# Kernel optimization log

Hardware: AMD Instinct MI355X
Metric: run time of the kernel (lower is better)

Reference implementation:

```python
import jax, jax.numpy as jnp
import numpy as np

H = 768      # hidden_size
R = 64       # lora_dim
E = 8        # n_experts
B, S = 8, 2048


def setup_inputs() -> dict:
    key = jax.random.key(0)
    ks = jax.random.split(key, 10)
    s_in = 1.0 / np.sqrt(H)
    s_r = 1.0 / np.sqrt(R)
    return {
        "x": jax.random.normal(ks[0], (B, S, H), dtype=jnp.float32),
        "enc_w": jax.random.uniform(ks[1], (H, R), jnp.float32, -s_in, s_in),
        "enc_b": jax.random.uniform(ks[2], (R,), jnp.float32, -s_in, s_in),
        "sw_w": jax.random.uniform(ks[3], (R, E), jnp.float32, -s_r, s_r),
        "sw_b": jax.random.uniform(ks[4], (E,), jnp.float32, -s_r, s_r),
        "w1": jax.random.uniform(ks[5], (E, H, R), jnp.float32, -s_in, s_in),
        "b1": jax.random.uniform(ks[6], (E, R), jnp.float32, -s_in, s_in),
        "w2": jax.random.uniform(ks[7], (E, R, H), jnp.float32, -s_r, s_r),
        "b2": jax.random.uniform(ks[8], (E, H), jnp.float32, -s_r, s_r),
    }


def reference(x, enc_w, enc_b, sw_w, sw_b, w1, b1, w2, b2):
    b, s, d = x.shape
    xt = x.reshape(-1, d)                                  # [T, H]
    # router: encoder -> switch -> softmax -> top-1
    x_enc = xt @ enc_w + enc_b                             # [T, R]
    route_prob = jax.nn.softmax(x_enc @ sw_w + sw_b, axis=-1)  # [T, E]
    route_prob_max = jnp.max(route_prob, axis=-1)          # [T]
    routes = jnp.argmax(route_prob, axis=-1)               # [T]
    onehot = jax.nn.one_hot(routes, E, dtype=xt.dtype)     # [T, E]
    # dense dispatch: per-(token, expert) LoRA bottleneck; masked combine
    h = jnp.einsum('td,edr->ter', xt, w1) + b1[None]       # [T, E, R]
    h = jax.nn.gelu(h, approximate=False)
    h = h * onehot[..., None]                              # zero non-routed
    out = jnp.einsum('ter,erd->td', h, w2) + onehot @ b2   # [T, H]
    out = out * route_prob_max[:, None]
    return out.reshape(b, s, d)
```

## Files before the change

kernel.cpp:

```cpp
#include <hip/hip_runtime.h>
#include <math.h>

#define HDIM 768
#define RDIM 64
#define NEXP 8
#define NTOK 16384

typedef _Float16 half8 __attribute__((ext_vector_type(8)));
typedef float float4_t __attribute__((ext_vector_type(4)));

__device__ __forceinline__ float gelu_exact(float v) {
    return 0.5f * v * (1.0f + erff(v * 0.70710678118654752440f));
}

__global__ __launch_bounds__(256) void prep_kernel(
    const float* __restrict__ w1, const float* __restrict__ w2,
    const float* __restrict__ enc_w, const float* __restrict__ enc_b,
    const float* __restrict__ sw_w, const float* __restrict__ sw_b,
    _Float16* __restrict__ w1t, _Float16* __restrict__ w2t,
    float* __restrict__ wrt, float* __restrict__ brr)
{
    const int wid = blockIdx.x * 4 + (threadIdx.x >> 6);
    const int lane = threadIdx.x & 63;
    if (wid < 768) {
        const int e = wid / 96, k0 = (wid % 96) * 8;
        half8 o;
        #pragma unroll
        for (int j = 0; j < 8; j++)
            o[j] = (_Float16)w1[((size_t)(e * HDIM + k0 + j)) * RDIM + lane];
        *(half8*)(w1t + ((size_t)(e * RDIM + lane)) * HDIM + k0) = o;
    } else if (wid < 1536) {
        const int id = wid - 768;
        const int e = id / 96, rem = id % 96;
        const int n = (rem >> 3) * 64 + lane, k0 = (rem & 7) * 8;
        half8 o;
        #pragma unroll
        for (int j = 0; j < 8; j++)
            o[j] = (_Float16)w2[((size_t)(e * RDIM + k0 + j)) * HDIM + n];
        *(half8*)(w2t + ((size_t)(e * HDIM + n)) * RDIM + k0) = o;
    } else if (wid < 1632) {
        const int k = (wid - 1536) * 8 + (lane >> 3);
        const int e = lane & 7;
        float s = 0.0f;
        #pragma unroll 16
        for (int r = 0; r < RDIM; r++)
            s += enc_w[(size_t)k * RDIM + r] * sw_w[r * NEXP + e];
        wrt[e * HDIM + k] = s;
    } else if (wid == 1632) {
        if (lane < NEXP) {
            float s = sw_b[lane];
            #pragma unroll 16
            for (int r = 0; r < RDIM; r++)
                s += enc_b[r] * sw_w[r * NEXP + lane];
            brr[lane] = s;
        }
    }
}

__global__ __launch_bounds__(256, 4) void router_kernel(
    const float* __restrict__ x, const float* __restrict__ wrt,
    const float* __restrict__ brr, float* __restrict__ pmax,
    int* __restrict__ counts, int* __restrict__ lists)
{
    __shared__ __align__(16) float wrl[NEXP][772];
    __shared__ int lcnt[NEXP], gbase[NEXP];

    const int tid = threadIdx.x;
    #pragma unroll
    for (int i0 = 0; i0 < 6; i0++) {
        const int i = tid + i0 * 256;
        const int e = i / 192, k4 = (i % 192) * 4;
        *(float4*)&wrl[e][k4] = *(const float4*)(wrt + e * HDIM + k4);
    }
    if (tid < NEXP) lcnt[tid] = 0;
    __syncthreads();

    const int wv = tid >> 6, lane = tid & 63;
    const int e = lane & 7, tslot = lane >> 3;
    const int tok = blockIdx.x * 32 + wv * 8 + tslot;
    const float* xrow = x + (size_t)tok * HDIM;

    float4_t acc4 = {0.0f, 0.0f, 0.0f, 0.0f};
    for (int k0 = 0; k0 < HDIM; k0 += 64) {
        float4 xv[16];
        #pragma unroll
        for (int u = 0; u < 16; u++)
            xv[u] = *(const float4*)(xrow + k0 + u * 4);
        #pragma unroll
        for (int u = 0; u < 16; u++) {
            const float4 w4 = *(const float4*)(&wrl[e][k0 + u * 4]);
            acc4[0] = fmaf(xv[u].x, w4.x, acc4[0]);
            acc4[1] = fmaf(xv[u].y, w4.y, acc4[1]);
            acc4[2] = fmaf(xv[u].z, w4.z, acc4[2]);
            acc4[3] = fmaf(xv[u].w, w4.w, acc4[3]);
        }
    }
    const float logit = (acc4[0] + acc4[1]) + (acc4[2] + acc4[3]) + brr[e];

    float m = logit; int am = e;
    #pragma unroll
    for (int d = 4; d >= 1; d >>= 1) {
        float om = __shfl_xor(m, d, 8);
        int oam  = __shfl_xor(am, d, 8);
        if (om > m || (om == m && oam < am)) { m = om; am = oam; }
    }
    float s = expf(logit - m);
    #pragma unroll
    for (int d = 1; d <= 4; d <<= 1) s += __shfl_xor(s, d, 8);

    int am_s = -1, lp_s = 0;
    if (e == 0) {
        pmax[tok] = 1.0f / s;
        am_s = am;
        lp_s = atomicAdd(&lcnt[am], 1);
    }
    __syncthreads();
    if (tid < NEXP) gbase[tid] = atomicAdd(&counts[tid * 32], lcnt[tid]);
    __syncthreads();
    if (am_s >= 0)
        lists[am_s * NTOK + gbase[am_s] + lp_s] = tok;
}

__global__ __launch_bounds__(256, 4) void mm1_kernel(
    const float* __restrict__ x, const _Float16* __restrict__ w1t,
    const float* __restrict__ b1, const int* __restrict__ counts,
    const int* __restrict__ lists, _Float16* __restrict__ h)
{
    __shared__ __align__(16) float part[4][16][68];

    const int e = blockIdx.x;
    const int cnt = counts[e * 32];
    const int tid = threadIdx.x;
    const int wv = tid >> 6, lane = tid & 63;
    const int q = lane >> 4, c = lane & 15;

    for (int st = blockIdx.y; st * 16 < cnt; st += gridDim.y) {
        const int base = st * 16;
        const int nt = cnt - base;
        const int tA = lists[e * NTOK + base + min(c, nt - 1)];
        const float* xrow = x + (size_t)tA * HDIM + wv * 192;
        const _Float16* wbase = w1t + ((size_t)(e * RDIM + c)) * HDIM + wv * 192 + q * 8;

        float4 xv[12];
        #pragma unroll
        for (int it = 0; it < 6; it++) {
            xv[2 * it]     = *(const float4*)(xrow + it * 32 + q * 8);
            xv[2 * it + 1] = *(const float4*)(xrow + it * 32 + q * 8 + 4);
        }

        float4_t acc[4] = {{0,0,0,0},{0,0,0,0},{0,0,0,0},{0,0,0,0}};
        #pragma unroll
        for (int it = 0; it < 6; it++) {
            const int k0 = it * 32;
            half8 a;
            a[0] = (_Float16)xv[2*it].x;   a[1] = (_Float16)xv[2*it].y;
            a[2] = (_Float16)xv[2*it].z;   a[3] = (_Float16)xv[2*it].w;
            a[4] = (_Float16)xv[2*it+1].x; a[5] = (_Float16)xv[2*it+1].y;
            a[6] = (_Float16)xv[2*it+1].z; a[7] = (_Float16)xv[2*it+1].w;
            #pragma unroll
            for (int nf = 0; nf < 4; nf++) {
                half8 b = *(const half8*)(wbase + (size_t)nf * 16 * HDIM + k0);
                acc[nf] = __builtin_amdgcn_mfma_f32_16x16x32_f16(a, b, acc[nf], 0, 0, 0);
            }
        }

        #pragma unroll
        for (int nf = 0; nf < 4; nf++)
            #pragma unroll
            for (int i = 0; i < 4; i++)
                part[wv][q * 4 + i][nf * 16 + c] = acc[nf][i];
        __syncthreads();

        #pragma unroll
        for (int j = 0; j < 4; j++) {
            const int idx = tid + 256 * j;
            const int row = idx >> 6, r = idx & 63;
            if (row < nt) {
                const int tok = lists[e * NTOK + base + row];
                float v = part[0][row][r] + part[1][row][r] + part[2][row][r]
                        + part[3][row][r] + b1[e * RDIM + r];
                h[(size_t)tok * RDIM + r] = (_Float16)gelu_exact(v);
            }
        }
        __syncthreads();
    }
}

__global__ __launch_bounds__(256, 3) void mm2_kernel(
    const _Float16* __restrict__ h, const _Float16* __restrict__ w2t,
    const float* __restrict__ b2, const float* __restrict__ pmax,
    const int* __restrict__ counts, const int* __restrict__ lists,
    float* __restrict__ out)
{
    const int e = blockIdx.x;
    const int cnt = counts[e * 32];
    const int wv = threadIdx.x >> 6, lane = threadIdx.x & 63;
    const int q = lane >> 4, c = lane & 15;

    const int task = blockIdx.y * 4 + wv;
    const int nch = task % 3;
    const int sidx = task / 3;

    for (int st = sidx; st * 16 < cnt; st += 128) {
        const int base = st * 16;
        const int nt = cnt - base;
        const int tA = lists[e * NTOK + base + min(c, nt - 1)];
        half8 a0 = *(const half8*)(h + (size_t)tA * RDIM + q * 8);
        half8 a1 = *(const half8*)(h + (size_t)tA * RDIM + 32 + q * 8);

        int tokv[4]; float pm[4]; bool ok[4];
        #pragma unroll
        for (int i = 0; i < 4; i++) {
            const int row = q * 4 + i;
            ok[i] = row < nt;
            tokv[i] = lists[e * NTOK + base + min(row, nt - 1)];
            pm[i] = pmax[tokv[i]];
        }

        #pragma unroll 4
        for (int nf = 0; nf < 16; nf++) {
            const int n = nch * 256 + nf * 16 + c;
            const _Float16* wrow = w2t + ((size_t)(e * HDIM + n)) * RDIM;
            half8 b0 = *(const half8*)(wrow + q * 8);
            half8 b1v = *(const half8*)(wrow + 32 + q * 8);
            float4_t acc = {0, 0, 0, 0};
            acc = __builtin_amdgcn_mfma_f32_16x16x32_f16(a0, b0, acc, 0, 0, 0);
            acc = __builtin_amdgcn_mfma_f32_16x16x32_f16(a1, b1v, acc, 0, 0, 0);
            const float b2v = b2[e * HDIM + n];
            #pragma unroll
            for (int i = 0; i < 4; i++) {
                if (ok[i])
                    out[(size_t)tokv[i] * HDIM + n] = (acc[i] + b2v) * pm[i];
            }
        }
    }
}

extern "C" void kernel_launch(void* const* d_in, const int* in_sizes, int n_in,
                              void* d_out, int out_size, void* d_ws, size_t ws_size,
                              hipStream_t stream) {
    const float* x     = (const float*)d_in[0];
    const float* enc_w = (const float*)d_in[1];
    const float* enc_b = (const float*)d_in[2];
    const float* sw_w  = (const float*)d_in[3];
    const float* sw_b  = (const float*)d_in[4];
    const float* w1    = (const float*)d_in[5];
    const float* b1    = (const float*)d_in[6];
    const float* w2    = (const float*)d_in[7];
    const float* b2    = (const float*)d_in[8];
    float* out = (float*)d_out;

    char* p = (char*)d_ws;
    int*      counts = (int*)p;
    float*    pmax   = (float*)(p + 1024);
    int*      lists  = (int*)(p + 66560);
    float*    wrt    = (float*)(p + 590848);
    float*    brr    = (float*)(p + 615424);
    _Float16* w1t    = (_Float16*)(p + 615680);
    _Float16* w2t    = (_Float16*)(p + 1402112);
    _Float16* h      = (_Float16*)(p + 2188544);

    hipMemsetAsync(d_ws, 0, 1024, stream);

    hipLaunchKernelGGL(prep_kernel, dim3(409), dim3(256), 0, stream,
                       w1, w2, enc_w, enc_b, sw_w, sw_b, w1t, w2t, wrt, brr);
    hipLaunchKernelGGL(router_kernel, dim3(NTOK / 32), dim3(256), 0, stream,
                       x, wrt, brr, pmax, counts, lists);
    hipLaunchKernelGGL(mm1_kernel, dim3(NEXP, 128), dim3(256), 0, stream,
                       x, w1t, b1, counts, lists, h);
    hipLaunchKernelGGL(mm2_kernel, dim3(NEXP, 96), dim3(256), 0, stream,
                       h, w2t, b2, pmax, counts, lists, out);
}
```

Measured before the change: 195.2 us.

## Fuse expert up and down projections into one kernel, restructure router reduction

Merges mm1 and mm2 into a single kernel: the GELU hidden tile for each 16-token block stays in shared memory and is consumed by the second MFMA projection, with each wave covering a 192-column slice of the output. This drops the global round trip for h and one kernel launch. The router is also reorganised so that 32 lanes split the K dimension of one token and compute all 8 expert logits with a shuffle reduction, which improves x load coalescing. In exchange, mm2 now has fewer blocks doing more serial work, plus extra syncthreads per tile.

```diff
diff --git a/kernel.cpp b/kernel.cpp
--- a/kernel.cpp
+++ b/kernel.cpp
@@ -73,60 +73,85 @@
         *(float4*)&wrl[e][k4] = *(const float4*)(wrt + e * HDIM + k4);
     }
     if (tid < NEXP) lcnt[tid] = 0;
+
+    const int wv = tid >> 6, lane = tid & 63;
+    const int h = lane & 31, hw = lane >> 5;
+
+    float br[8];
+    #pragma unroll
+    for (int e = 0; e < 8; e++) br[e] = brr[e];
     __syncthreads();
 
-    const int wv = tid >> 6, lane = tid & 63;
-    const int e = lane & 7, tslot = lane >> 3;
-    const int tok = blockIdx.x * 32 + wv * 8 + tslot;
-    const float* xrow = x + (size_t)tok * HDIM;
-
-    float4_t acc4 = {0.0f, 0.0f, 0.0f, 0.0f};
-    for (int k0 = 0; k0 < HDIM; k0 += 64) {
-        float4 xv[16];
-        #pragma unroll
-        for (int u = 0; u < 16; u++)
-            xv[u] = *(const float4*)(xrow + k0 + u * 4);
-        #pragma unroll
-        for (int u = 0; u < 16; u++) {
-            const float4 w4 = *(const float4*)(&wrl[e][k0 + u * 4]);
-            acc4[0] = fmaf(xv[u].x, w4.x, acc4[0]);
-            acc4[1] = fmaf(xv[u].y, w4.y, acc4[1]);
-            acc4[2] = fmaf(xv[u].z, w4.z, acc4[2]);
-            acc4[3] = fmaf(xv[u].w, w4.w, acc4[3]);
-        }
-    }
-    const float logit = (acc4[0] + acc4[1]) + (acc4[2] + acc4[3]) + brr[e];
-
-    float m = logit; int am = e;
-    #pragma unroll
-    for (int d = 4; d >= 1; d >>= 1) {
-        float om = __shfl_xor(m, d, 8);
-        int oam  = __shfl_xor(am, d, 8);
-        if (om > m || (om == m && oam < am)) { m = om; am = oam; }
-    }
-    float s = expf(logit - m);
-    #pragma unroll
-    for (int d = 1; d <= 4; d <<= 1) s += __shfl_xor(s, d, 8);
-
-    int am_s = -1, lp_s = 0;
-    if (e == 0) {
-        pmax[tok] = 1.0f / s;
-        am_s = am;
-        lp_s = atomicAdd(&lcnt[am], 1);
+    int amv[2], lpv[2], tkv[2];
+    #pragma unroll
+    for (int it = 0; it < 2; it++) {
+        const int tok = blockIdx.x * 16 + it * 8 + wv * 2 + hw;
+        const float* xrow = x + (size_t)tok * HDIM;
+        float4 xv[6];
+        #pragma unroll
+        for (int g = 0; g < 6; g++)
+            xv[g] = *(const float4*)(xrow + g * 128 + h * 4);
+
+        float acc[8];
+        #pragma unroll
+        for (int e = 0; e < 8; e++) acc[e] = 0.0f;
+        #pragma unroll
+        for (int e = 0; e < 8; e++) {
+            #pragma unroll
+            for (int g = 0; g < 6; g++) {
+                const float4 w4 = *(const float4*)&wrl[e][g * 128 + h * 4];
+                acc[e] = fmaf(xv[g].x, w4.x, acc[e]);
+                acc[e] = fmaf(xv[g].y, w4.y, acc[e]);
+                acc[e] = fmaf(xv[g].z, w4.z, acc[e]);
+                acc[e] = fmaf(xv[g].w, w4.w, acc[e]);
+            }
+        }
+        #pragma unroll
+        for (int d = 1; d < 32; d <<= 1) {
+            #pragma unroll
+            for (int e = 0; e < 8; e++)
+                acc[e] += __shfl_xor(acc[e], d);
+        }
+        float lg[8];
+        lg[0] = acc[0] + br[0];
+        float m = lg[0]; int am = 0;
+        #pragma unroll
+        for (int e = 1; e < 8; e++) {
+            lg[e] = acc[e] + br[e];
+            if (lg[e] > m) { m = lg[e]; am = e; }
+        }
+        float s = 0.0f;
+        #pragma unroll
+        for (int e = 0; e < 8; e++) s += expf(lg[e] - m);
+
+        amv[it] = -1;
+        if (h == 0) {
+            pmax[tok] = 1.0f / s;
+            amv[it] = am;
+            lpv[it] = atomicAdd(&lcnt[am], 1);
+            tkv[it] = tok;
+        }
     }
     __syncthreads();
     if (tid < NEXP) gbase[tid] = atomicAdd(&counts[tid * 32], lcnt[tid]);
     __syncthreads();
-    if (am_s >= 0)
-        lists[am_s * NTOK + gbase[am_s] + lp_s] = tok;
-}
-
-__global__ __launch_bounds__(256, 4) void mm1_kernel(
+    #pragma unroll
+    for (int it = 0; it < 2; it++)
+        if (amv[it] >= 0)
+            lists[amv[it] * NTOK + gbase[amv[it]] + lpv[it]] = tkv[it];
+}
+
+__global__ __launch_bounds__(256, 4) void mm12_kernel(
     const float* __restrict__ x, const _Float16* __restrict__ w1t,
-    const float* __restrict__ b1, const int* __restrict__ counts,
-    const int* __restrict__ lists, _Float16* __restrict__ h)
+    const float* __restrict__ b1, const _Float16* __restrict__ w2t,
+    const float* __restrict__ b2, const float* __restrict__ pmax,
+    const int* __restrict__ counts, const int* __restrict__ lists,
+    float* __restrict__ out)
 {
     __shared__ __align__(16) float part[4][16][68];
+    __shared__ __align__(16) _Float16 hl[16][72];
+    __shared__ float pml[16];
+    __shared__ int tkl[16];
 
     const int e = blockIdx.x;
     const int cnt = counts[e * 32];
@@ -143,20 +168,20 @@
 
         float4 xv[12];
         #pragma unroll
-        for (int it = 0; it < 6; it++) {
-            xv[2 * it]     = *(const float4*)(xrow + it * 32 + q * 8);
-            xv[2 * it + 1] = *(const float4*)(xrow + it * 32 + q * 8 + 4);
+        for (int itk = 0; itk < 6; itk++) {
+            xv[2 * itk]     = *(const float4*)(xrow + itk * 32 + q * 8);
+            xv[2 * itk + 1] = *(const float4*)(xrow + itk * 32 + q * 8 + 4);
         }
 
         float4_t acc[4] = {{0,0,0,0},{0,0,0,0},{0,0,0,0},{0,0,0,0}};
         #pragma unroll
-        for (int it = 0; it < 6; it++) {
-            const int k0 = it * 32;
+        for (int itk = 0; itk < 6; itk++) {
+            const int k0 = itk * 32;
             half8 a;
-            a[0] = (_Float16)xv[2*it].x;   a[1] = (_Float16)xv[2*it].y;
-            a[2] = (_Float16)xv[2*it].z;   a[3] = (_Float16)xv[2*it].w;
-            a[4] = (_Float16)xv[2*it+1].x; a[5] = (_Float16)xv[2*it+1].y;
-            a[6] = (_Float16)xv[2*it+1].z; a[7] = (_Float16)xv[2*it+1].w;
+            a[0] = (_Float16)xv[2*itk].x;   a[1] = (_Float16)xv[2*itk].y;
+            a[2] = (_Float16)xv[2*itk].z;   a[3] = (_Float16)xv[2*itk].w;
+            a[4] = (_Float16)xv[2*itk+1].x; a[5] = (_Float16)xv[2*itk+1].y;
+            a[6] = (_Float16)xv[2*itk+1].z; a[7] = (_Float16)xv[2*itk+1].w;
             #pragma unroll
             for (int nf = 0; nf < 4; nf++) {
                 half8 b = *(const half8*)(wbase + (size_t)nf * 16 * HDIM + k0);
@@ -164,6 +189,12 @@
             }
         }
 
+        if (tid < 16) {
+            const int t = lists[e * NTOK + base + min(tid, nt - 1)];
+            tkl[tid] = t;
+            pml[tid] = pmax[t];
+        }
+
         #pragma unroll
         for (int nf = 0; nf < 4; nf++)
             #pragma unroll
@@ -175,64 +206,39 @@
         for (int j = 0; j < 4; j++) {
             const int idx = tid + 256 * j;
             const int row = idx >> 6, r = idx & 63;
-            if (row < nt) {
-                const int tok = lists[e * NTOK + base + row];
-                float v = part[0][row][r] + part[1][row][r] + part[2][row][r]
-                        + part[3][row][r] + b1[e * RDIM + r];
-                h[(size_t)tok * RDIM + r] = (_Float16)gelu_exact(v);
-            }
+            float v = part[0][row][r] + part[1][row][r] + part[2][row][r]
+                    + part[3][row][r] + b1[e * RDIM + r];
+            hl[row][r] = (_Float16)gelu_exact(v);
         }
         __syncthreads();
-    }
-}
-
-__global__ __launch_bounds__(256, 3) void mm2_kernel(
-    const _Float16* __restrict__ h, const _Float16* __restrict__ w2t,
-    const float* __restrict__ b2, const float* __restrict__ pmax,
-    const int* __restrict__ counts, const int* __restrict__ lists,
-    float* __restrict__ out)
-{
-    const int e = blockIdx.x;
-    const int cnt = counts[e * 32];
-    const int wv = threadIdx.x >> 6, lane = threadIdx.x & 63;
-    const int q = lane >> 4, c = lane & 15;
-
-    const int task = blockIdx.y * 4 + wv;
-    const int nch = task % 3;
-    const int sidx = task / 3;
-
-    for (int st = sidx; st * 16 < cnt; st += 128) {
-        const int base = st * 16;
-        const int nt = cnt - base;
-        const int tA = lists[e * NTOK + base + min(c, nt - 1)];
-        half8 a0 = *(const half8*)(h + (size_t)tA * RDIM + q * 8);
-        half8 a1 = *(const half8*)(h + (size_t)tA * RDIM + 32 + q * 8);
-
+
+        half8 a0 = *(const half8*)&hl[c][q * 8];
+        half8 a1 = *(const half8*)&hl[c][32 + q * 8];
         int tokv[4]; float pm[4]; bool ok[4];
         #pragma unroll
         for (int i = 0; i < 4; i++) {
             const int row = q * 4 + i;
             ok[i] = row < nt;
-            tokv[i] = lists[e * NTOK + base + min(row, nt - 1)];
-            pm[i] = pmax[tokv[i]];
-        }
-
+            tokv[i] = tkl[row];
+            pm[i] = pml[row];
+        }
         #pragma unroll 4
-        for (int nf = 0; nf < 16; nf++) {
-            const int n = nch * 256 + nf * 16 + c;
+        for (int nf = 0; nf < 12; nf++) {
+            const int n = wv * 192 + nf * 16 + c;
             const _Float16* wrow = w2t + ((size_t)(e * HDIM + n)) * RDIM;
-            half8 b0 = *(const half8*)(wrow + q * 8);
+            half8 b0  = *(const half8*)(wrow + q * 8);
             half8 b1v = *(const half8*)(wrow + 32 + q * 8);
-            float4_t acc = {0, 0, 0, 0};
-            acc = __builtin_amdgcn_mfma_f32_16x16x32_f16(a0, b0, acc, 0, 0, 0);
-            acc = __builtin_amdgcn_mfma_f32_16x16x32_f16(a1, b1v, acc, 0, 0, 0);
+            float4_t acc2 = {0, 0, 0, 0};
+            acc2 = __builtin_amdgcn_mfma_f32_16x16x32_f16(a0, b0, acc2, 0, 0, 0);
+            acc2 = __builtin_amdgcn_mfma_f32_16x16x32_f16(a1, b1v, acc2, 0, 0, 0);
             const float b2v = b2[e * HDIM + n];
             #pragma unroll
             for (int i = 0; i < 4; i++) {
                 if (ok[i])
-                    out[(size_t)tokv[i] * HDIM + n] = (acc[i] + b2v) * pm[i];
+                    out[(size_t)tokv[i] * HDIM + n] = (acc2[i] + b2v) * pm[i];
             }
         }
+        __syncthreads();
     }
 }
 
@@ -258,16 +264,13 @@
     float*    brr    = (float*)(p + 615424);
     _Float16* w1t    = (_Float16*)(p + 615680);
     _Float16* w2t    = (_Float16*)(p + 1402112);
-    _Float16* h      = (_Float16*)(p + 2188544);
 
     hipMemsetAsync(d_ws, 0, 1024, stream);
 
     hipLaunchKernelGGL(prep_kernel, dim3(409), dim3(256), 0, stream,
                        w1, w2, enc_w, enc_b, sw_w, sw_b, w1t, w2t, wrt, brr);
-    hipLaunchKernelGGL(router_kernel, dim3(NTOK / 32), dim3(256), 0, stream,
+    hipLaunchKernelGGL(router_kernel, dim3(NTOK / 16), dim3(256), 0, stream,
                        x, wrt, brr, pmax, counts, lists);
-    hipLaunchKernelGGL(mm1_kernel, dim3(NEXP, 128), dim3(256), 0, stream,
-                       x, w1t, b1, counts, lists, h);
-    hipLaunchKernelGGL(mm2_kernel, dim3(NEXP, 96), dim3(256), 0, stream,
-                       h, w2t, b2, pmax, counts, lists, out);
-}
+    hipLaunchKernelGGL(mm12_kernel, dim3(NEXP, 128), dim3(256), 0, stream,
+                       x, w1t, b1, w2t, b2, pmax, counts, lists, out);
+}
```

Measured after the change: 194.8 us. About the same (-0.2%).

## Restructure router so half-waves cooperatively read token rows coalesced

Applied to the files above, without the earlier changes.

The router kernel now assigns each token to 32 lanes that each load a contiguous float4 slice of the row, so the x reads are coalesced across lanes. Before, each lane streamed a whole row by itself for one expert, and eight lanes read the same row redundantly. Each lane now computes partial dot products for all 8 experts and reduces them with xor shuffles across the half-wave. Each block handles 16 tokens over two iterations, so the grid doubles. This trades uncoalesced, redundant row reads for more shuffle reductions and more blocks, each of which reloads the router weights into LDS.

```diff
diff --git a/kernel.cpp b/kernel.cpp
--- a/kernel.cpp
+++ b/kernel.cpp
@@ -73,52 +73,72 @@
         *(float4*)&wrl[e][k4] = *(const float4*)(wrt + e * HDIM + k4);
     }
     if (tid < NEXP) lcnt[tid] = 0;
+
+    const int wv = tid >> 6, lane = tid & 63;
+    const int h = lane & 31, hw = lane >> 5;
+
+    float br[8];
+    #pragma unroll
+    for (int e = 0; e < 8; e++) br[e] = brr[e];
     __syncthreads();
 
-    const int wv = tid >> 6, lane = tid & 63;
-    const int e = lane & 7, tslot = lane >> 3;
-    const int tok = blockIdx.x * 32 + wv * 8 + tslot;
-    const float* xrow = x + (size_t)tok * HDIM;
-
-    float4_t acc4 = {0.0f, 0.0f, 0.0f, 0.0f};
-    for (int k0 = 0; k0 < HDIM; k0 += 64) {
-        float4 xv[16];
-        #pragma unroll
-        for (int u = 0; u < 16; u++)
-            xv[u] = *(const float4*)(xrow + k0 + u * 4);
-        #pragma unroll
-        for (int u = 0; u < 16; u++) {
-            const float4 w4 = *(const float4*)(&wrl[e][k0 + u * 4]);
-            acc4[0] = fmaf(xv[u].x, w4.x, acc4[0]);
-            acc4[1] = fmaf(xv[u].y, w4.y, acc4[1]);
-            acc4[2] = fmaf(xv[u].z, w4.z, acc4[2]);
-            acc4[3] = fmaf(xv[u].w, w4.w, acc4[3]);
-        }
-    }
-    const float logit = (acc4[0] + acc4[1]) + (acc4[2] + acc4[3]) + brr[e];
-
-    float m = logit; int am = e;
-    #pragma unroll
-    for (int d = 4; d >= 1; d >>= 1) {
-        float om = __shfl_xor(m, d, 8);
-        int oam  = __shfl_xor(am, d, 8);
-        if (om > m || (om == m && oam < am)) { m = om; am = oam; }
-    }
-    float s = expf(logit - m);
-    #pragma unroll
-    for (int d = 1; d <= 4; d <<= 1) s += __shfl_xor(s, d, 8);
-
-    int am_s = -1, lp_s = 0;
-    if (e == 0) {
-        pmax[tok] = 1.0f / s;
-        am_s = am;
-        lp_s = atomicAdd(&lcnt[am], 1);
+    int amv[2], lpv[2], tkv[2];
+    #pragma unroll
+    for (int it = 0; it < 2; it++) {
+        const int tok = blockIdx.x * 16 + it * 8 + wv * 2 + hw;
+        const float* xrow = x + (size_t)tok * HDIM;
+        float4 xv[6];
+        #pragma unroll
+        for (int g = 0; g < 6; g++)
+            xv[g] = *(const float4*)(xrow + g * 128 + h * 4);
+
+        float acc[8];
+        #pragma unroll
+        for (int e = 0; e < 8; e++) acc[e] = 0.0f;
+        #pragma unroll
+        for (int e = 0; e < 8; e++) {
+            #pragma unroll
+            for (int g = 0; g < 6; g++) {
+                const float4 w4 = *(const float4*)&wrl[e][g * 128 + h * 4];
+                acc[e] = fmaf(xv[g].x, w4.x, acc[e]);
+                acc[e] = fmaf(xv[g].y, w4.y, acc[e]);
+                acc[e] = fmaf(xv[g].z, w4.z, acc[e]);
+                acc[e] = fmaf(xv[g].w, w4.w, acc[e]);
+            }
+        }
+        #pragma unroll
+        for (int d = 1; d < 32; d <<= 1) {
+            #pragma unroll
+            for (int e = 0; e < 8; e++)
+                acc[e] += __shfl_xor(acc[e], d);
+        }
+        float lg[8];
+        lg[0] = acc[0] + br[0];
+        float m = lg[0]; int am = 0;
+        #pragma unroll
+        for (int e = 1; e < 8; e++) {
+            lg[e] = acc[e] + br[e];
+            if (lg[e] > m) { m = lg[e]; am = e; }
+        }
+        float s = 0.0f;
+        #pragma unroll
+        for (int e = 0; e < 8; e++) s += expf(lg[e] - m);
+
+        amv[it] = -1;
+        if (h == 0) {
+            pmax[tok] = 1.0f / s;
+            amv[it] = am;
+            lpv[it] = atomicAdd(&lcnt[am], 1);
+            tkv[it] = tok;
+        }
     }
     __syncthreads();
     if (tid < NEXP) gbase[tid] = atomicAdd(&counts[tid * 32], lcnt[tid]);
     __syncthreads();
-    if (am_s >= 0)
-        lists[am_s * NTOK + gbase[am_s] + lp_s] = tok;
+    #pragma unroll
+    for (int it = 0; it < 2; it++)
+        if (amv[it] >= 0)
+            lists[amv[it] * NTOK + gbase[amv[it]] + lpv[it]] = tkv[it];
 }
 
 __global__ __launch_bounds__(256, 4) void mm1_kernel(
@@ -264,7 +284,7 @@
 
     hipLaunchKernelGGL(prep_kernel, dim3(409), dim3(256), 0, stream,
                        w1, w2, enc_w, enc_b, sw_w, sw_b, w1t, w2t, wrt, brr);
-    hipLaunchKernelGGL(router_kernel, dim3(NTOK / 32), dim3(256), 0, stream,
+    hipLaunchKernelGGL(router_kernel, dim3(NTOK / 16), dim3(256), 0, stream,
                        x, wrt, brr, pmax, counts, lists);
     hipLaunchKernelGGL(mm1_kernel, dim3(NEXP, 128), dim3(256), 0, stream,
                        x, w1t, b1, counts, lists, h);
```

After: 187.3 us. 1.04x faster.
